# Kernel optimization log

Measured on AMD Instinct MI355X. Metric: run time of the kernel, lower is better.

## Reference

```python
import jax, jax.numpy as jnp
import numpy as np

B, S, H, E, T, L = 128, 1024, 512, 512, 64, 128


def setup_inputs() -> dict:
    key = jax.random.key(0)
    ks = jax.random.split(key, 20)
    s = 0.02
    inp = {
        "sent_lengths": jax.random.randint(ks[0], (B,), 1, S, dtype=jnp.int32),
        "output_length": T,
        "decoder_input": jax.random.normal(ks[1], (B, E), jnp.float32),
        "h0": jax.random.normal(ks[2], (B, H), jnp.float32),
        "c0": jax.random.normal(ks[3], (B, H), jnp.float32),
        "context": jax.random.normal(ks[4], (B, S, H), jnp.float32),
        "cur_labels": jax.random.randint(ks[5], (B, T), 0, L, dtype=jnp.int32),
        "cur_max_nsymbs": jax.random.randint(ks[6], (B,), 0, 10, dtype=jnp.int32),
        # parameters
        "label_emb": jax.random.normal(ks[7], (L, E), jnp.float32) * s,
        "W_ih": jax.random.normal(ks[8], (4 * H, E), jnp.float32) * s,
        "b_ih": jnp.zeros((4 * H,), jnp.float32),
        "W_hh": jax.random.normal(ks[9], (4 * H, H), jnp.float32) * s,
        "b_hh": jnp.zeros((4 * H,), jnp.float32),
        "W_ho": jax.random.normal(ks[10], (H, 2 * H), jnp.float32) * s,
        "b_ho": jnp.zeros((H,), jnp.float32),
        "W_attn_in": jax.random.normal(ks[11], (H, H), jnp.float32) * s,
        "b_attn_in": jnp.zeros((H,), jnp.float32),
        "W_attn_ctx": jax.random.normal(ks[12], (H, H), jnp.float32) * s,
        "b_attn_ctx": jnp.zeros((H,), jnp.float32),
        "V": jax.random.uniform(ks[13], (H,), jnp.float32, -1.0, 1.0),
        "W_out": jax.random.normal(ks[14], (L, 2 * H + E), jnp.float32) * s,
        "b_out": jnp.zeros((L,), jnp.float32),
    }
    # padding_idx row of the label embedding is zero (torch nn.Embedding semantics)
    inp["label_emb"] = inp["label_emb"].at[0].set(0.0)
    return inp


def _decode(output_length, decoder_input, h0, c0, context, cur_labels,
            label_emb, W_ih, b_ih, W_hh, b_hh, W_ho, b_ho,
            W_attn_in, b_attn_in, W_attn_ctx, b_attn_ctx, V, W_out, b_out):
    # Precompute the 1x1-conv context projection once (identical math to per-step conv).
    ctx = jnp.einsum("bsh,gh->bsg", context, W_attn_ctx) + b_attn_ctx  # [B,S,H]

    # Teacher-forced input sequence: x_0 = decoder_input, x_i = emb(labels[:, i-1]).
    emb = label_emb[cur_labels]                     # [B,T,E]
    xs = jnp.concatenate(
        [decoder_input[None], jnp.swapaxes(emb, 0, 1)[: output_length - 1]], axis=0
    )                                               # [T,B,E]

    def step(carry, x):
        h, c = carry
        gates = x @ W_ih.T + b_ih + h @ W_hh.T + b_hh          # [B,4H]
        i_g, f_g, g_g, o_g = jnp.split(gates, 4, axis=1)
        c_t = jax.nn.sigmoid(f_g) * c + jax.nn.sigmoid(i_g) * jnp.tanh(g_g)
        h_lstm = jax.nn.sigmoid(o_g) * jnp.tanh(c_t)            # [B,H]
        # pointer attention
        inp = h_lstm @ W_attn_in.T + b_attn_in                  # [B,H]
        att = jnp.einsum("bsh,h->bs", jnp.tanh(inp[:, None, :] + ctx), V)
        alpha = jax.nn.softmax(att, axis=-1)                    # [B,S]
        weighted = jnp.einsum("bs,bsh->bh", alpha, ctx)         # [B,H]
        hidden_t = jnp.tanh(jnp.concatenate([weighted, h_lstm], 1) @ W_ho.T + b_ho)
        out = jnp.concatenate([hidden_t, weighted, x], 1) @ W_out.T + b_out  # [B,L]
        return (hidden_t, c_t), out

    (h_f, c_f), outs = jax.lax.scan(step, (h0, c0), xs)  # outs [T,B,L]
    outputs = jnp.transpose(outs, (1, 0, 2))             # [B,T,L]
    preds = jnp.argmax(outputs, axis=-1)                 # [B,T]
    return outputs, preds, h_f, c_f


def reference(sent_lengths, output_length, decoder_input, h0, c0, context,
              cur_labels, cur_max_nsymbs, label_emb, W_ih, b_ih, W_hh, b_hh,
              W_ho, b_ho, W_attn_in, b_attn_in, W_attn_ctx, b_attn_ctx, V,
              W_out, b_out):
    # cur_batch_len = len(sent_lengths) == B, so hidden slicing is a no-op here.
    # cur_max_nsymbs unused (constrained_decoding=None path).
    return _decode(output_length, decoder_input, h0, c0, context, cur_labels,
                   label_emb, W_ih, b_ih, W_hh, b_hh, W_ho, b_ho,
                   W_attn_in, b_attn_in, W_attn_ctx, b_attn_ctx, V, W_out, b_out)
```

## Files before the change

kernel.cpp:

```cpp
#include <hip/hip_runtime.h>
#include <hip/hip_bf16.h>
#include <math.h>

#define B_ 128
#define S_ 1024
#define H_ 512
#define E_ 512
#define T_ 64
#define L_ 128
#define G4H 2048

typedef __attribute__((ext_vector_type(8))) short bf16x8;
typedef __attribute__((ext_vector_type(4))) float f32x4;

__device__ inline float sigmoidf_(float x) { return 1.f / (1.f + expf(-x)); }
__device__ inline float fast_tanhf_(float x) {
    float e = __expf(2.f * x);
    return 1.f - 2.f / (e + 1.f);
}
__device__ inline unsigned f2bf1(float f) {
    unsigned u = __float_as_uint(f);
    return (u + 0x7fffu + ((u >> 16) & 1u)) >> 16;
}

#define LDP 40
__global__ __launch_bounds__(256) void gemm_split(
    const float* __restrict__ A, int lda,
    const float* __restrict__ W, int ldw,
    const float* __restrict__ bias,
    const float* __restrict__ Cinit, int ldci,
    float* __restrict__ C, int ldc,
    int K, int act, int perm)
{
    __shared__ unsigned short Ah[128 * LDP];
    __shared__ unsigned short Al[128 * LDP];
    __shared__ unsigned short Bh[128 * LDP];
    __shared__ unsigned short Bl[128 * LDP];
    const int n0 = blockIdx.x * 128;
    const int m0 = blockIdx.y * 128;
    const int t = threadIdx.x;
    const int lane = t & 63, wv = t >> 6;
    const int wr = wv >> 1, wc = wv & 1;
    const int row = t >> 1, koff = (t & 1) * 16;

    f32x4 acc[4][4] = {};

    for (int kt = 0; kt < K; kt += 32) {
        float av[16], wvv[16];
        {
            const float* ap = A + (size_t)(m0 + row) * lda + kt + koff;
            const float* wp = W + (size_t)(n0 + row) * ldw + kt + koff;
#pragma unroll
            for (int q = 0; q < 4; ++q) {
                *reinterpret_cast<float4*>(&av[q * 4]) = *reinterpret_cast<const float4*>(ap + q * 4);
                *reinterpret_cast<float4*>(&wvv[q * 4]) = *reinterpret_cast<const float4*>(wp + q * 4);
            }
        }
        unsigned short ah[16], al[16], bh[16], bl[16];
#pragma unroll
        for (int e = 0; e < 16; ++e) {
            unsigned ha = f2bf1(av[e]);
            float hf = __uint_as_float(ha << 16);
            ah[e] = (unsigned short)ha;
            al[e] = (unsigned short)f2bf1(av[e] - hf);
            unsigned hw = f2bf1(wvv[e]);
            float hwf = __uint_as_float(hw << 16);
            bh[e] = (unsigned short)hw;
            bl[e] = (unsigned short)f2bf1(wvv[e] - hwf);
        }
        __syncthreads();
        *reinterpret_cast<uint4*>(&Ah[row * LDP + koff])     = *reinterpret_cast<uint4*>(&ah[0]);
        *reinterpret_cast<uint4*>(&Ah[row * LDP + koff + 8]) = *reinterpret_cast<uint4*>(&ah[8]);
        *reinterpret_cast<uint4*>(&Al[row * LDP + koff])     = *reinterpret_cast<uint4*>(&al[0]);
        *reinterpret_cast<uint4*>(&Al[row * LDP + koff + 8]) = *reinterpret_cast<uint4*>(&al[8]);
        *reinterpret_cast<uint4*>(&Bh[row * LDP + koff])     = *reinterpret_cast<uint4*>(&bh[0]);
        *reinterpret_cast<uint4*>(&Bh[row * LDP + koff + 8]) = *reinterpret_cast<uint4*>(&bh[8]);
        *reinterpret_cast<uint4*>(&Bl[row * LDP + koff])     = *reinterpret_cast<uint4*>(&bl[0]);
        *reinterpret_cast<uint4*>(&Bl[row * LDP + koff + 8]) = *reinterpret_cast<uint4*>(&bl[8]);
        __syncthreads();

        bf16x8 fah[4], fal[4], fbh[4], fbl[4];
        const int kq = (lane >> 4) * 8;
#pragma unroll
        for (int i = 0; i < 4; ++i) {
            const int ar = wr * 64 + i * 16 + (lane & 15);
            const int br = wc * 64 + i * 16 + (lane & 15);
            fah[i] = *reinterpret_cast<const bf16x8*>(&Ah[ar * LDP + kq]);
            fal[i] = *reinterpret_cast<const bf16x8*>(&Al[ar * LDP + kq]);
            fbh[i] = *reinterpret_cast<const bf16x8*>(&Bh[br * LDP + kq]);
            fbl[i] = *reinterpret_cast<const bf16x8*>(&Bl[br * LDP + kq]);
        }
#pragma unroll
        for (int i = 0; i < 4; ++i)
#pragma unroll
            for (int j = 0; j < 4; ++j) {
                acc[i][j] = __builtin_amdgcn_mfma_f32_16x16x32_bf16(fah[i], fbh[j], acc[i][j], 0, 0, 0);
                acc[i][j] = __builtin_amdgcn_mfma_f32_16x16x32_bf16(fal[i], fbh[j], acc[i][j], 0, 0, 0);
                acc[i][j] = __builtin_amdgcn_mfma_f32_16x16x32_bf16(fah[i], fbl[j], acc[i][j], 0, 0, 0);
            }
    }

#pragma unroll
    for (int i = 0; i < 4; ++i)
#pragma unroll
        for (int j = 0; j < 4; ++j) {
            const int n = n0 + wc * 64 + j * 16 + (lane & 15);
            const float bs = bias ? bias[n] : 0.f;
#pragma unroll
            for (int r = 0; r < 4; ++r) {
                const int m = m0 + wr * 64 + i * 16 + (lane >> 4) * 4 + r;
                float v = acc[i][j][r] + bs;
                if (Cinit) v += Cinit[(size_t)m * ldci + n];
                if (act == 1) v = tanhf(v);
                size_t crow;
                if (perm) { int bb = m & 127, tt = m >> 7; crow = ((size_t)bb * T_ + tt) * ldc; }
                else crow = (size_t)m * ldc;
                C[crow + n] = v;
            }
        }
}

__global__ __launch_bounds__(128) void k_perm(
    const float* __restrict__ W_ih, const float* __restrict__ W_hh,
    const float* __restrict__ b_ih, const float* __restrict__ b_hh,
    float* __restrict__ Wip, float* __restrict__ Whp, float* __restrict__ bp)
{
    int rp = blockIdx.x;
    int h = rp >> 2, g = rp & 3;
    int src = g * 512 + h;
    int t = threadIdx.x;
    const float4* si = reinterpret_cast<const float4*>(W_ih + (size_t)src * 512);
    const float4* sh = reinterpret_cast<const float4*>(W_hh + (size_t)src * 512);
    float4* di = reinterpret_cast<float4*>(Wip + (size_t)rp * 512);
    float4* dh = reinterpret_cast<float4*>(Whp + (size_t)rp * 512);
    di[t] = si[t];
    dh[t] = sh[t];
    if (t == 0) bp[rp] = b_ih[src] + b_hh[src];
}

__global__ __launch_bounds__(256) void k_gateslstm(
    const float* __restrict__ hbuf,
    const float* __restrict__ Whp,
    const float* __restrict__ xproj_t,
    float* __restrict__ cbuf,
    float* __restrict__ hlstm)
{
    __shared__ float As[16][32];
    __shared__ float Ws[16][64];
    const int n0 = blockIdx.x * 64;
    const int m0 = blockIdx.y * 32;
    const int t = threadIdx.x;
    const int tx = t & 15;
    const int ty = t >> 4;
    const int alr = t >> 3, alk = (t & 7) * 2;
    const int wlr = t >> 2, wlk = (t & 3) * 4;

    float acc[2][4] = {};

    for (int k0 = 0; k0 < 512; k0 += 16) {
        float2 a2 = *reinterpret_cast<const float2*>(hbuf + (size_t)(m0 + alr) * 512 + k0 + alk);
        float4 w4 = *reinterpret_cast<const float4*>(Whp + (size_t)(n0 + wlr) * 512 + k0 + wlk);
        __syncthreads();
        As[alk + 0][alr] = a2.x; As[alk + 1][alr] = a2.y;
        Ws[wlk + 0][wlr] = w4.x; Ws[wlk + 1][wlr] = w4.y;
        Ws[wlk + 2][wlr] = w4.z; Ws[wlk + 3][wlr] = w4.w;
        __syncthreads();
#pragma unroll
        for (int kk = 0; kk < 16; ++kk) {
            float a[2], b[4];
            a[0] = As[kk][ty * 2]; a[1] = As[kk][ty * 2 + 1];
#pragma unroll
            for (int j = 0; j < 4; ++j) b[j] = Ws[kk][tx * 4 + j];
#pragma unroll
            for (int i = 0; i < 2; ++i)
#pragma unroll
                for (int j = 0; j < 4; ++j) acc[i][j] = fmaf(a[i], b[j], acc[i][j]);
        }
    }

    const int h = (n0 >> 2) + tx;
#pragma unroll
    for (int i = 0; i < 2; ++i) {
        const int b = m0 + ty * 2 + i;
        float4 xp = *reinterpret_cast<const float4*>(xproj_t + (size_t)b * G4H + n0 + tx * 4);
        float ig = sigmoidf_(acc[i][0] + xp.x);
        float fg = sigmoidf_(acc[i][1] + xp.y);
        float gg = tanhf(acc[i][2] + xp.z);
        float og = sigmoidf_(acc[i][3] + xp.w);
        float c = fg * cbuf[(size_t)b * 512 + h] + ig * gg;
        cbuf[(size_t)b * 512 + h] = c;
        hlstm[(size_t)b * 512 + h] = og * tanhf(c);
    }
}

__global__ __launch_bounds__(256) void gemm_stepk(
    const float* __restrict__ A, int lda,
    const float* __restrict__ W, int ldw,
    float* __restrict__ P, int N, int Kc)
{
    __shared__ float As[16][128];
    __shared__ float Ws[16][64];
    const int n0 = blockIdx.x * 64;
    const int k0 = blockIdx.y * Kc;
    const int t = threadIdx.x;
    const int tx = t & 15;
    const int ty = t >> 4;
    const int ar = t >> 1, akq = (t & 1) * 8;
    const int wr = t >> 2, wkq = (t & 3) * 4;

    float acc[8][4] = {};

    for (int kb = 0; kb < Kc; kb += 16) {
        float4 a0 = *reinterpret_cast<const float4*>(A + (size_t)ar * lda + k0 + kb + akq);
        float4 a1 = *reinterpret_cast<const float4*>(A + (size_t)ar * lda + k0 + kb + akq + 4);
        float4 w0 = *reinterpret_cast<const float4*>(W + (size_t)(n0 + wr) * ldw + k0 + kb + wkq);
        __syncthreads();
        As[akq + 0][ar] = a0.x; As[akq + 1][ar] = a0.y; As[akq + 2][ar] = a0.z; As[akq + 3][ar] = a0.w;
        As[akq + 4][ar] = a1.x; As[akq + 5][ar] = a1.y; As[akq + 6][ar] = a1.z; As[akq + 7][ar] = a1.w;
        Ws[wkq + 0][wr] = w0.x; Ws[wkq + 1][wr] = w0.y; Ws[wkq + 2][wr] = w0.z; Ws[wkq + 3][wr] = w0.w;
        __syncthreads();
#pragma unroll
        for (int kk = 0; kk < 16; ++kk) {
            float a[8], b[4];
#pragma unroll
            for (int i = 0; i < 8; ++i) a[i] = As[kk][ty * 8 + i];
#pragma unroll
            for (int j = 0; j < 4; ++j) b[j] = Ws[kk][tx * 4 + j];
#pragma unroll
            for (int i = 0; i < 8; ++i)
#pragma unroll
                for (int j = 0; j < 4; ++j) acc[i][j] = fmaf(a[i], b[j], acc[i][j]);
        }
    }

#pragma unroll
    for (int i = 0; i < 8; ++i) {
        const int m = ty * 8 + i;
#pragma unroll
        for (int j = 0; j < 4; ++j)
            P[((size_t)blockIdx.y * 128 + m) * N + n0 + tx * 4 + j] = acc[i][j];
    }
}

__global__ __launch_bounds__(256) void k_who(
    const float* __restrict__ pm, const float* __restrict__ pl,
    const float* __restrict__ pw, const float* __restrict__ hlstm,
    const float* __restrict__ W_ho,
    float* __restrict__ P, float* __restrict__ hist_t)
{
    __shared__ float As[16][128];
    __shared__ float Ws[16][64];
    __shared__ float eql[128][4];
    const int n0 = blockIdx.x * 64;
    const int k0 = blockIdx.y * 128;
    const int t = threadIdx.x;
    const int tx = t & 15;
    const int ty = t >> 4;
    const int ar = t >> 1, akq = (t & 1) * 8;
    const int wr = t >> 2, wkq = (t & 3) * 4;
    const bool merge_side = (k0 < 512);
    const bool writer = (blockIdx.x == 0) && merge_side;

    if (merge_side && t < 128) {
        float m0 = pm[4 * t], m1 = pm[4 * t + 1], m2 = pm[4 * t + 2], m3 = pm[4 * t + 3];
        float M = fmaxf(fmaxf(m0, m1), fmaxf(m2, m3));
        float e0 = __expf(m0 - M), e1 = __expf(m1 - M), e2 = __expf(m2 - M), e3 = __expf(m3 - M);
        float Lt = e0 * pl[4 * t] + e1 * pl[4 * t + 1] + e2 * pl[4 * t + 2] + e3 * pl[4 * t + 3];
        float inv = 1.f / Lt;
        eql[t][0] = e0 * inv; eql[t][1] = e1 * inv; eql[t][2] = e2 * inv; eql[t][3] = e3 * inv;
    }
    __syncthreads();

    float acc[8][4] = {};

    for (int kb = 0; kb < 128; kb += 16) {
        float av[8];
        const int kg = k0 + kb + akq;
        if (merge_side) {
            float4 p0a = *reinterpret_cast<const float4*>(pw + ((size_t)(4 * ar + 0) * 512) + kg);
            float4 p0b = *reinterpret_cast<const float4*>(pw + ((size_t)(4 * ar + 0) * 512) + kg + 4);
            float4 p1a = *reinterpret_cast<const float4*>(pw + ((size_t)(4 * ar + 1) * 512) + kg);
            float4 p1b = *reinterpret_cast<const float4*>(pw + ((size_t)(4 * ar + 1) * 512) + kg + 4);
            float4 p2a = *reinterpret_cast<const float4*>(pw + ((size_t)(4 * ar + 2) * 512) + kg);
            float4 p2b = *reinterpret_cast<const float4*>(pw + ((size_t)(4 * ar + 2) * 512) + kg + 4);
            float4 p3a = *reinterpret_cast<const float4*>(pw + ((size_t)(4 * ar + 3) * 512) + kg);
            float4 p3b = *reinterpret_cast<const float4*>(pw + ((size_t)(4 * ar + 3) * 512) + kg + 4);
            float q0 = eql[ar][0], q1 = eql[ar][1], q2 = eql[ar][2], q3 = eql[ar][3];
            av[0] = q0 * p0a.x + q1 * p1a.x + q2 * p2a.x + q3 * p3a.x;
            av[1] = q0 * p0a.y + q1 * p1a.y + q2 * p2a.y + q3 * p3a.y;
            av[2] = q0 * p0a.z + q1 * p1a.z + q2 * p2a.z + q3 * p3a.z;
            av[3] = q0 * p0a.w + q1 * p1a.w + q2 * p2a.w + q3 * p3a.w;
            av[4] = q0 * p0b.x + q1 * p1b.x + q2 * p2b.x + q3 * p3b.x;
            av[5] = q0 * p0b.y + q1 * p1b.y + q2 * p2b.y + q3 * p3b.y;
            av[6] = q0 * p0b.z + q1 * p1b.z + q2 * p2b.z + q3 * p3b.z;
            av[7] = q0 * p0b.w + q1 * p1b.w + q2 * p2b.w + q3 * p3b.w;
            if (writer) {
                *reinterpret_cast<float4*>(hist_t + (size_t)ar * 1024 + 512 + kg) = *reinterpret_cast<float4*>(&av[0]);
                *reinterpret_cast<float4*>(hist_t + (size_t)ar * 1024 + 512 + kg + 4) = *reinterpret_cast<float4*>(&av[4]);
            }
        } else {
            *reinterpret_cast<float4*>(&av[0]) = *reinterpret_cast<const float4*>(hlstm + (size_t)ar * 512 + kg - 512);
            *reinterpret_cast<float4*>(&av[4]) = *reinterpret_cast<const float4*>(hlstm + (size_t)ar * 512 + kg - 512 + 4);
        }
        float4 w0 = *reinterpret_cast<const float4*>(W_ho + (size_t)(n0 + wr) * 1024 + k0 + kb + wkq);
        __syncthreads();
        As[akq + 0][ar] = av[0]; As[akq + 1][ar] = av[1]; As[akq + 2][ar] = av[2]; As[akq + 3][ar] = av[3];
        As[akq + 4][ar] = av[4]; As[akq + 5][ar] = av[5]; As[akq + 6][ar] = av[6]; As[akq + 7][ar] = av[7];
        Ws[wkq + 0][wr] = w0.x; Ws[wkq + 1][wr] = w0.y; Ws[wkq + 2][wr] = w0.z; Ws[wkq + 3][wr] = w0.w;
        __syncthreads();
#pragma unroll
        for (int kk = 0; kk < 16; ++kk) {
            float a[8], b[4];
#pragma unroll
            for (int i = 0; i < 8; ++i) a[i] = As[kk][ty * 8 + i];
#pragma unroll
            for (int j = 0; j < 4; ++j) b[j] = Ws[kk][tx * 4 + j];
#pragma unroll
            for (int i = 0; i < 8; ++i)
#pragma unroll
                for (int j = 0; j < 4; ++j) acc[i][j] = fmaf(a[i], b[j], acc[i][j]);
        }
    }

#pragma unroll
    for (int i = 0; i < 8; ++i) {
        const int m = ty * 8 + i;
#pragma unroll
        for (int j = 0; j < 4; ++j)
            P[((size_t)blockIdx.y * 128 + m) * 512 + n0 + tx * 4 + j] = acc[i][j];
    }
}

__global__ void k_embed(const float* __restrict__ dec_in, const int* __restrict__ labels,
                        const float* __restrict__ emb, float* __restrict__ X)
{
    size_t total = (size_t)T_ * B_ * E_;
    for (size_t i = (size_t)blockIdx.x * blockDim.x + threadIdx.x; i < total;
         i += (size_t)gridDim.x * blockDim.x) {
        int e = (int)(i % E_);
        int b = (int)((i / E_) % B_);
        int t = (int)(i / ((size_t)E_ * B_));
        float v;
        if (t == 0) v = dec_in[b * E_ + e];
        else {
            int lab = labels[b * T_ + (t - 1)];
            v = emb[(size_t)lab * E_ + e];
        }
        X[i] = v;
    }
}

__global__ void k_init(const float* __restrict__ h0, const float* __restrict__ c0,
                       float* __restrict__ hbuf, float* __restrict__ cbuf)
{
    int i = blockIdx.x * blockDim.x + threadIdx.x;
    hbuf[i] = h0[i];
    cbuf[i] = c0[i];
}

__global__ __launch_bounds__(512) void k_attn(const float* __restrict__ ctx,
    const float* __restrict__ Pa, const float* __restrict__ b_ain,
    const float* __restrict__ Vv,
    float* __restrict__ pm, float* __restrict__ pl, float* __restrict__ pw)
{
    int blk = blockIdx.x;
    int b = blk >> 2, q = blk & 3;
    int tid = threadIdx.x, lane = tid & 63, wv = tid >> 6;

    __shared__ float inp_sh[512];
    inp_sh[tid] = Pa[(size_t)b * 512 + tid]
                + Pa[(size_t)(128 + b) * 512 + tid]
                + Pa[(size_t)(256 + b) * 512 + tid]
                + Pa[(size_t)(384 + b) * 512 + tid]
                + b_ain[tid];
    __syncthreads();

    float inpr[8], vr[8];
    {
        const float4* v4 = reinterpret_cast<const float4*>(Vv) + lane * 2;
        *(float4*)&vr[0] = v4[0];   *(float4*)&vr[4] = v4[1];
#pragma unroll
        for (int k = 0; k < 8; ++k) inpr[k] = inp_sh[lane * 8 + k];
    }
    const float* cbase = ctx + (size_t)b * S_ * H_ + (size_t)(q * 256) * H_;

    float m = -INFINITY, l = 0.f, w[8] = {};
    for (int si = 0; si < 32; ++si) {
        int s = wv * 32 + si;
        const float4* cp = reinterpret_cast<const float4*>(cbase + (size_t)s * H_) + lane * 2;
        float c8[8];
        *(float4*)&c8[0] = cp[0]; *(float4*)&c8[4] = cp[1];
        float t = 0.f;
#pragma unroll
        for (int k = 0; k < 8; ++k) t = fmaf(fast_tanhf_(inpr[k] + c8[k]), vr[k], t);
#pragma unroll
        for (int off = 32; off > 0; off >>= 1) t += __shfl_xor(t, off);
        float mn = fmaxf(m, t);
        float sc = __expf(m - mn);
        float p  = __expf(t - mn);
        l = l * sc + p;
#pragma unroll
        for (int k = 0; k < 8; ++k) w[k] = w[k] * sc + p * c8[k];
        m = mn;
    }

    __shared__ float wl[8 * 512];
    __shared__ float ml[8], ll[8];
#pragma unroll
    for (int k = 0; k < 8; ++k) wl[wv * 512 + lane * 8 + k] = w[k];
    if (lane == 0) { ml[wv] = m; ll[wv] = l; }
    __syncthreads();

    float M = ml[0];
#pragma unroll
    for (int u = 1; u < 8; ++u) M = fmaxf(M, ml[u]);
    float lt = 0.f, wt = 0.f;
#pragma unroll
    for (int u = 0; u < 8; ++u) {
        float e = __expf(ml[u] - M);
        lt += e * ll[u];
        wt += e * wl[u * 512 + tid];
    }
    if (tid == 0) { pm[blk] = M; pl[blk] = lt; }
    pw[(size_t)blk * 512 + tid] = wt;
}

__global__ __launch_bounds__(256) void k_whofin(const float* __restrict__ Po,
    const float* __restrict__ b_ho, float* __restrict__ hbuf, float* __restrict__ hist_t)
{
    int i = blockIdx.x * blockDim.x + threadIdx.x;
    int b = i >> 9, h = i & 511;
    float v = b_ho[h];
#pragma unroll
    for (int ks = 0; ks < 8; ++ks) v += Po[((size_t)ks * 128 + b) * 512 + h];
    v = tanhf(v);
    hbuf[i] = v;
    hist_t[(size_t)b * 1024 + h] = v;
}

__global__ __launch_bounds__(128) void k_argmax(const float* __restrict__ outp,
                                                float* __restrict__ preds)
{
    int row = blockIdx.x;
    int tid = threadIdx.x;
    float v = outp[(size_t)row * L_ + tid];
    int idx = tid;
#pragma unroll
    for (int off = 32; off > 0; off >>= 1) {
        float ov = __shfl_xor(v, off);
        int oi = __shfl_xor(idx, off);
        if (ov > v || (ov == v && oi < idx)) { v = ov; idx = oi; }
    }
    __shared__ float sv[2];
    __shared__ int si[2];
    if ((tid & 63) == 0) { sv[tid >> 6] = v; si[tid >> 6] = idx; }
    __syncthreads();
    if (tid == 0) {
        float v0 = sv[0], v1 = sv[1];
        int i0 = si[0], i1 = si[1];
        int r = (v1 > v0 || (v1 == v0 && i1 < i0)) ? i1 : i0;
        preds[row] = (float)r;
    }
}

__global__ void k_final(const float* __restrict__ hbuf, const float* __restrict__ cbuf,
                        float* __restrict__ hf, float* __restrict__ cf)
{
    int i = blockIdx.x * blockDim.x + threadIdx.x;
    hf[i] = hbuf[i];
    cf[i] = cbuf[i];
}

extern "C" void kernel_launch(void* const* d_in, const int* in_sizes, int n_in,
                              void* d_out, int out_size, void* d_ws, size_t ws_size,
                              hipStream_t stream)
{
    const float* dec_in  = (const float*)d_in[2];
    const float* h0      = (const float*)d_in[3];
    const float* c0      = (const float*)d_in[4];
    const float* context = (const float*)d_in[5];
    const int*   labels  = (const int*)d_in[6];
    const float* emb     = (const float*)d_in[8];
    const float* W_ih    = (const float*)d_in[9];
    const float* b_ih    = (const float*)d_in[10];
    const float* W_hh    = (const float*)d_in[11];
    const float* b_hh    = (const float*)d_in[12];
    const float* W_ho    = (const float*)d_in[13];
    const float* b_ho    = (const float*)d_in[14];
    const float* W_ain   = (const float*)d_in[15];
    const float* b_ain   = (const float*)d_in[16];
    const float* W_actx  = (const float*)d_in[17];
    const float* b_actx  = (const float*)d_in[18];
    const float* Vv      = (const float*)d_in[19];
    const float* W_out   = (const float*)d_in[20];
    const float* b_out   = (const float*)d_in[21];

    float* ws = (float*)d_ws;
    float* X     = ws; ws += (size_t)T_ * B_ * E_;
    float* xproj = ws; ws += (size_t)T_ * B_ * G4H;
    float* xout  = ws; ws += (size_t)T_ * B_ * L_;
    float* ctx   = ws; ws += (size_t)B_ * S_ * H_;
    float* hist  = ws; ws += (size_t)T_ * B_ * 1024;
    float* Wip   = ws; ws += (size_t)G4H * 512;
    float* Whp   = ws; ws += (size_t)G4H * 512;
    float* bp    = ws; ws += G4H;
    float* Pa    = ws; ws += (size_t)4 * B_ * H_;
    float* Po    = ws; ws += (size_t)8 * B_ * H_;
    float* cbuf  = ws; ws += (size_t)B_ * H_;
    float* hbuf  = ws; ws += (size_t)B_ * H_;
    float* hlstm = ws; ws += (size_t)B_ * H_;
    float* pm    = ws; ws += 512;
    float* pl    = ws; ws += 512;
    float* pw    = ws; ws += (size_t)512 * 512;

    float* out_logits = (float*)d_out;
    float* out_preds  = out_logits + (size_t)B_ * T_ * L_;
    float* out_hf     = out_preds + (size_t)B_ * T_;
    float* out_cf     = out_hf + (size_t)B_ * H_;

    k_embed<<<2048, 256, 0, stream>>>(dec_in, labels, emb, X);
    k_init<<<256, 256, 0, stream>>>(h0, c0, hbuf, cbuf);
    k_perm<<<G4H, 128, 0, stream>>>(W_ih, W_hh, b_ih, b_hh, Wip, Whp, bp);
    gemm_split<<<dim3(16, 64), 256, 0, stream>>>(X, E_, Wip, E_, bp, nullptr, 0,
                                                 xproj, G4H, E_, 0, 0);
    gemm_split<<<dim3(1, 64), 256, 0, stream>>>(X, E_, W_out + 1024, 1536, b_out, nullptr, 0,
                                                xout, L_, E_, 0, 0);
    gemm_split<<<dim3(4, 1024), 256, 0, stream>>>(context, H_, W_actx, H_, b_actx, nullptr, 0,
                                                  ctx, H_, H_, 0, 0);

    for (int t = 0; t < T_; ++t) {
        float* hist_t = hist + (size_t)t * B_ * 1024;
        k_gateslstm<<<dim3(32, 4), 256, 0, stream>>>(hbuf, Whp,
                                                     xproj + (size_t)t * B_ * G4H,
                                                     cbuf, hlstm);
        gemm_stepk<<<dim3(8, 4), 256, 0, stream>>>(hlstm, H_, W_ain, H_, Pa, H_, 128);
        k_attn<<<512, 512, 0, stream>>>(ctx, Pa, b_ain, Vv, pm, pl, pw);
        k_who<<<dim3(8, 8), 256, 0, stream>>>(pm, pl, pw, hlstm, W_ho, Po, hist_t);
        k_whofin<<<256, 256, 0, stream>>>(Po, b_ho, hbuf, hist_t);
    }

    gemm_split<<<dim3(1, 64), 256, 0, stream>>>(hist, 1024, W_out, 1536, nullptr,
                                                xout, L_, out_logits, L_, 1024, 0, 1);
    k_argmax<<<B_ * T_, 128, 0, stream>>>(out_logits, out_preds);
    k_final<<<256, 256, 0, stream>>>(hbuf, cbuf, out_hf, out_cf);
}
```

Baseline: 8.182 ms.

## Register-prefetch next tiles in GEMMs and split attention into eight S-chunks

Adds register double-buffering to gemm_split, the LSTM gates kernel, gemm_stepk and k_who, so the global loads for the next K tile are issued before the current tile's compute. The attention kernel is split into 8 sequence chunks per batch row instead of 4, giving 1024 blocks with 16 positions per wave and a prefetch of the next context row. The W_ho merge side now combines 8 partial softmax results, and the workspace buffers are resized to match. In exchange there is more partial-result traffic and merge work in k_who, plus higher register pressure from the prefetched values.

```diff
diff --git a/kernel.cpp b/kernel.cpp
--- a/kernel.cpp
+++ b/kernel.cpp
@@ -9,6 +9,7 @@
 #define T_ 64
 #define L_ 128
 #define G4H 2048
+#define QS 8
 
 typedef __attribute__((ext_vector_type(8))) short bf16x8;
 typedef __attribute__((ext_vector_type(4))) float f32x4;
@@ -45,17 +46,18 @@
 
     f32x4 acc[4][4] = {};
 
+    float av[16], wvv[16];
+    {
+        const float* ap = A + (size_t)(m0 + row) * lda + koff;
+        const float* wp = W + (size_t)(n0 + row) * ldw + koff;
+#pragma unroll
+        for (int q = 0; q < 4; ++q) {
+            *reinterpret_cast<float4*>(&av[q * 4]) = *reinterpret_cast<const float4*>(ap + q * 4);
+            *reinterpret_cast<float4*>(&wvv[q * 4]) = *reinterpret_cast<const float4*>(wp + q * 4);
+        }
+    }
+
     for (int kt = 0; kt < K; kt += 32) {
-        float av[16], wvv[16];
-        {
-            const float* ap = A + (size_t)(m0 + row) * lda + kt + koff;
-            const float* wp = W + (size_t)(n0 + row) * ldw + kt + koff;
-#pragma unroll
-            for (int q = 0; q < 4; ++q) {
-                *reinterpret_cast<float4*>(&av[q * 4]) = *reinterpret_cast<const float4*>(ap + q * 4);
-                *reinterpret_cast<float4*>(&wvv[q * 4]) = *reinterpret_cast<const float4*>(wp + q * 4);
-            }
-        }
         unsigned short ah[16], al[16], bh[16], bl[16];
 #pragma unroll
         for (int e = 0; e < 16; ++e) {
@@ -78,6 +80,16 @@
         *reinterpret_cast<uint4*>(&Bl[row * LDP + koff])     = *reinterpret_cast<uint4*>(&bl[0]);
         *reinterpret_cast<uint4*>(&Bl[row * LDP + koff + 8]) = *reinterpret_cast<uint4*>(&bl[8]);
         __syncthreads();
+
+        if (kt + 32 < K) {
+            const float* ap = A + (size_t)(m0 + row) * lda + kt + 32 + koff;
+            const float* wp = W + (size_t)(n0 + row) * ldw + kt + 32 + koff;
+#pragma unroll
+            for (int q = 0; q < 4; ++q) {
+                *reinterpret_cast<float4*>(&av[q * 4]) = *reinterpret_cast<const float4*>(ap + q * 4);
+                *reinterpret_cast<float4*>(&wvv[q * 4]) = *reinterpret_cast<const float4*>(wp + q * 4);
+            }
+        }
 
         bf16x8 fah[4], fal[4], fbh[4], fbl[4];
         const int kq = (lane >> 4) * 8;
@@ -157,14 +169,19 @@
 
     float acc[2][4] = {};
 
+    float2 pa = *reinterpret_cast<const float2*>(hbuf + (size_t)(m0 + alr) * 512 + alk);
+    float4 pv = *reinterpret_cast<const float4*>(Whp + (size_t)(n0 + wlr) * 512 + wlk);
+
     for (int k0 = 0; k0 < 512; k0 += 16) {
-        float2 a2 = *reinterpret_cast<const float2*>(hbuf + (size_t)(m0 + alr) * 512 + k0 + alk);
-        float4 w4 = *reinterpret_cast<const float4*>(Whp + (size_t)(n0 + wlr) * 512 + k0 + wlk);
-        __syncthreads();
-        As[alk + 0][alr] = a2.x; As[alk + 1][alr] = a2.y;
-        Ws[wlk + 0][wlr] = w4.x; Ws[wlk + 1][wlr] = w4.y;
-        Ws[wlk + 2][wlr] = w4.z; Ws[wlk + 3][wlr] = w4.w;
-        __syncthreads();
+        __syncthreads();
+        As[alk + 0][alr] = pa.x; As[alk + 1][alr] = pa.y;
+        Ws[wlk + 0][wlr] = pv.x; Ws[wlk + 1][wlr] = pv.y;
+        Ws[wlk + 2][wlr] = pv.z; Ws[wlk + 3][wlr] = pv.w;
+        __syncthreads();
+        if (k0 + 16 < 512) {
+            pa = *reinterpret_cast<const float2*>(hbuf + (size_t)(m0 + alr) * 512 + k0 + 16 + alk);
+            pv = *reinterpret_cast<const float4*>(Whp + (size_t)(n0 + wlr) * 512 + k0 + 16 + wlk);
+        }
 #pragma unroll
         for (int kk = 0; kk < 16; ++kk) {
             float a[2], b[4];
@@ -210,15 +227,21 @@
 
     float acc[8][4] = {};
 
+    float4 a0 = *reinterpret_cast<const float4*>(A + (size_t)ar * lda + k0 + akq);
+    float4 a1 = *reinterpret_cast<const float4*>(A + (size_t)ar * lda + k0 + akq + 4);
+    float4 w0 = *reinterpret_cast<const float4*>(W + (size_t)(n0 + wr) * ldw + k0 + wkq);
+
     for (int kb = 0; kb < Kc; kb += 16) {
-        float4 a0 = *reinterpret_cast<const float4*>(A + (size_t)ar * lda + k0 + kb + akq);
-        float4 a1 = *reinterpret_cast<const float4*>(A + (size_t)ar * lda + k0 + kb + akq + 4);
-        float4 w0 = *reinterpret_cast<const float4*>(W + (size_t)(n0 + wr) * ldw + k0 + kb + wkq);
         __syncthreads();
         As[akq + 0][ar] = a0.x; As[akq + 1][ar] = a0.y; As[akq + 2][ar] = a0.z; As[akq + 3][ar] = a0.w;
         As[akq + 4][ar] = a1.x; As[akq + 5][ar] = a1.y; As[akq + 6][ar] = a1.z; As[akq + 7][ar] = a1.w;
         Ws[wkq + 0][wr] = w0.x; Ws[wkq + 1][wr] = w0.y; Ws[wkq + 2][wr] = w0.z; Ws[wkq + 3][wr] = w0.w;
         __syncthreads();
+        if (kb + 16 < Kc) {
+            a0 = *reinterpret_cast<const float4*>(A + (size_t)ar * lda + k0 + kb + 16 + akq);
+            a1 = *reinterpret_cast<const float4*>(A + (size_t)ar * lda + k0 + kb + 16 + akq + 4);
+            w0 = *reinterpret_cast<const float4*>(W + (size_t)(n0 + wr) * ldw + k0 + kb + 16 + wkq);
+        }
 #pragma unroll
         for (int kk = 0; kk < 16; ++kk) {
             float a[8], b[4];
@@ -250,7 +273,7 @@
 {
     __shared__ float As[16][128];
     __shared__ float Ws[16][64];
-    __shared__ float eql[128][4];
+    __shared__ float eql[128][QS];
     const int n0 = blockIdx.x * 64;
     const int k0 = blockIdx.y * 128;
     const int t = threadIdx.x;
@@ -262,38 +285,39 @@
     const bool writer = (blockIdx.x == 0) && merge_side;
 
     if (merge_side && t < 128) {
-        float m0 = pm[4 * t], m1 = pm[4 * t + 1], m2 = pm[4 * t + 2], m3 = pm[4 * t + 3];
-        float M = fmaxf(fmaxf(m0, m1), fmaxf(m2, m3));
-        float e0 = __expf(m0 - M), e1 = __expf(m1 - M), e2 = __expf(m2 - M), e3 = __expf(m3 - M);
-        float Lt = e0 * pl[4 * t] + e1 * pl[4 * t + 1] + e2 * pl[4 * t + 2] + e3 * pl[4 * t + 3];
+        float mq[QS], eq[QS];
+        float M = -INFINITY;
+#pragma unroll
+        for (int q = 0; q < QS; ++q) { mq[q] = pm[QS * t + q]; M = fmaxf(M, mq[q]); }
+        float Lt = 0.f;
+#pragma unroll
+        for (int q = 0; q < QS; ++q) { eq[q] = __expf(mq[q] - M); Lt += eq[q] * pl[QS * t + q]; }
         float inv = 1.f / Lt;
-        eql[t][0] = e0 * inv; eql[t][1] = e1 * inv; eql[t][2] = e2 * inv; eql[t][3] = e3 * inv;
+#pragma unroll
+        for (int q = 0; q < QS; ++q) eql[t][q] = eq[q] * inv;
     }
     __syncthreads();
 
     float acc[8][4] = {};
-
-    for (int kb = 0; kb < 128; kb += 16) {
-        float av[8];
+    float av[8];
+    float4 w0;
+
+    auto load_stage = [&](int kb) {
         const int kg = k0 + kb + akq;
         if (merge_side) {
-            float4 p0a = *reinterpret_cast<const float4*>(pw + ((size_t)(4 * ar + 0) * 512) + kg);
-            float4 p0b = *reinterpret_cast<const float4*>(pw + ((size_t)(4 * ar + 0) * 512) + kg + 4);
-            float4 p1a = *reinterpret_cast<const float4*>(pw + ((size_t)(4 * ar + 1) * 512) + kg);
-            float4 p1b = *reinterpret_cast<const float4*>(pw + ((size_t)(4 * ar + 1) * 512) + kg + 4);
-            float4 p2a = *reinterpret_cast<const float4*>(pw + ((size_t)(4 * ar + 2) * 512) + kg);
-            float4 p2b = *reinterpret_cast<const float4*>(pw + ((size_t)(4 * ar + 2) * 512) + kg + 4);
-            float4 p3a = *reinterpret_cast<const float4*>(pw + ((size_t)(4 * ar + 3) * 512) + kg);
-            float4 p3b = *reinterpret_cast<const float4*>(pw + ((size_t)(4 * ar + 3) * 512) + kg + 4);
-            float q0 = eql[ar][0], q1 = eql[ar][1], q2 = eql[ar][2], q3 = eql[ar][3];
-            av[0] = q0 * p0a.x + q1 * p1a.x + q2 * p2a.x + q3 * p3a.x;
-            av[1] = q0 * p0a.y + q1 * p1a.y + q2 * p2a.y + q3 * p3a.y;
-            av[2] = q0 * p0a.z + q1 * p1a.z + q2 * p2a.z + q3 * p3a.z;
-            av[3] = q0 * p0a.w + q1 * p1a.w + q2 * p2a.w + q3 * p3a.w;
-            av[4] = q0 * p0b.x + q1 * p1b.x + q2 * p2b.x + q3 * p3b.x;
-            av[5] = q0 * p0b.y + q1 * p1b.y + q2 * p2b.y + q3 * p3b.y;
-            av[6] = q0 * p0b.z + q1 * p1b.z + q2 * p2b.z + q3 * p3b.z;
-            av[7] = q0 * p0b.w + q1 * p1b.w + q2 * p2b.w + q3 * p3b.w;
+#pragma unroll
+            for (int e = 0; e < 8; ++e) av[e] = 0.f;
+#pragma unroll
+            for (int q = 0; q < QS; ++q) {
+                const float* pr = pw + (size_t)(QS * ar + q) * 512 + kg;
+                float4 pa = *reinterpret_cast<const float4*>(pr);
+                float4 pb = *reinterpret_cast<const float4*>(pr + 4);
+                float qw = eql[ar][q];
+                av[0] = fmaf(qw, pa.x, av[0]); av[1] = fmaf(qw, pa.y, av[1]);
+                av[2] = fmaf(qw, pa.z, av[2]); av[3] = fmaf(qw, pa.w, av[3]);
+                av[4] = fmaf(qw, pb.x, av[4]); av[5] = fmaf(qw, pb.y, av[5]);
+                av[6] = fmaf(qw, pb.z, av[6]); av[7] = fmaf(qw, pb.w, av[7]);
+            }
             if (writer) {
                 *reinterpret_cast<float4*>(hist_t + (size_t)ar * 1024 + 512 + kg) = *reinterpret_cast<float4*>(&av[0]);
                 *reinterpret_cast<float4*>(hist_t + (size_t)ar * 1024 + 512 + kg + 4) = *reinterpret_cast<float4*>(&av[4]);
@@ -302,12 +326,18 @@
             *reinterpret_cast<float4*>(&av[0]) = *reinterpret_cast<const float4*>(hlstm + (size_t)ar * 512 + kg - 512);
             *reinterpret_cast<float4*>(&av[4]) = *reinterpret_cast<const float4*>(hlstm + (size_t)ar * 512 + kg - 512 + 4);
         }
-        float4 w0 = *reinterpret_cast<const float4*>(W_ho + (size_t)(n0 + wr) * 1024 + k0 + kb + wkq);
+        w0 = *reinterpret_cast<const float4*>(W_ho + (size_t)(n0 + wr) * 1024 + k0 + kb + wkq);
+    };
+
+    load_stage(0);
+
+    for (int kb = 0; kb < 128; kb += 16) {
         __syncthreads();
         As[akq + 0][ar] = av[0]; As[akq + 1][ar] = av[1]; As[akq + 2][ar] = av[2]; As[akq + 3][ar] = av[3];
         As[akq + 4][ar] = av[4]; As[akq + 5][ar] = av[5]; As[akq + 6][ar] = av[6]; As[akq + 7][ar] = av[7];
         Ws[wkq + 0][wr] = w0.x; Ws[wkq + 1][wr] = w0.y; Ws[wkq + 2][wr] = w0.z; Ws[wkq + 3][wr] = w0.w;
         __syncthreads();
+        if (kb + 16 < 128) load_stage(kb + 16);
 #pragma unroll
         for (int kk = 0; kk < 16; ++kk) {
             float a[8], b[4];
@@ -364,7 +394,7 @@
     float* __restrict__ pm, float* __restrict__ pl, float* __restrict__ pw)
 {
     int blk = blockIdx.x;
-    int b = blk >> 2, q = blk & 3;
+    int b = blk >> 3, q = blk & 7;
     int tid = threadIdx.x, lane = tid & 63, wv = tid >> 6;
 
     __shared__ float inp_sh[512];
@@ -382,14 +412,19 @@
 #pragma unroll
         for (int k = 0; k < 8; ++k) inpr[k] = inp_sh[lane * 8 + k];
     }
-    const float* cbase = ctx + (size_t)b * S_ * H_ + (size_t)(q * 256) * H_;
+    const float* sp = ctx + ((size_t)b * S_ + q * 128 + wv * 16) * H_ + lane * 8;
 
     float m = -INFINITY, l = 0.f, w[8] = {};
-    for (int si = 0; si < 32; ++si) {
-        int s = wv * 32 + si;
-        const float4* cp = reinterpret_cast<const float4*>(cbase + (size_t)s * H_) + lane * 2;
+    float4 c0 = *reinterpret_cast<const float4*>(sp);
+    float4 c1 = *reinterpret_cast<const float4*>(sp + 4);
+    for (int si = 0; si < 16; ++si) {
+        float4 u0 = c0, u1 = c1;
+        if (si < 15) {
+            c0 = *reinterpret_cast<const float4*>(sp + (size_t)(si + 1) * H_);
+            c1 = *reinterpret_cast<const float4*>(sp + (size_t)(si + 1) * H_ + 4);
+        }
         float c8[8];
-        *(float4*)&c8[0] = cp[0]; *(float4*)&c8[4] = cp[1];
+        *(float4*)&c8[0] = u0; *(float4*)&c8[4] = u1;
         float t = 0.f;
 #pragma unroll
         for (int k = 0; k < 8; ++k) t = fmaf(fast_tanhf_(inpr[k] + c8[k]), vr[k], t);
@@ -509,9 +544,9 @@
     float* cbuf  = ws; ws += (size_t)B_ * H_;
     float* hbuf  = ws; ws += (size_t)B_ * H_;
     float* hlstm = ws; ws += (size_t)B_ * H_;
-    float* pm    = ws; ws += 512;
-    float* pl    = ws; ws += 512;
-    float* pw    = ws; ws += (size_t)512 * 512;
+    float* pm    = ws; ws += (size_t)B_ * QS;
+    float* pl    = ws; ws += (size_t)B_ * QS;
+    float* pw    = ws; ws += (size_t)B_ * QS * 512;
 
     float* out_logits = (float*)d_out;
     float* out_preds  = out_logits + (size_t)B_ * T_ * L_;
@@ -534,7 +569,7 @@
                                                      xproj + (size_t)t * B_ * G4H,
                                                      cbuf, hlstm);
         gemm_stepk<<<dim3(8, 4), 256, 0, stream>>>(hlstm, H_, W_ain, H_, Pa, H_, 128);
-        k_attn<<<512, 512, 0, stream>>>(ctx, Pa, b_ain, Vv, pm, pl, pw);
+        k_attn<<<B_ * QS, 512, 0, stream>>>(ctx, Pa, b_ain, Vv, pm, pl, pw);
         k_who<<<dim3(8, 8), 256, 0, stream>>>(pm, pl, pw, hlstm, W_ho, Po, hist_t);
         k_whofin<<<256, 256, 0, stream>>>(Po, b_ho, hbuf, hist_t);
     }
```

Measured after the change: 7.470 ms. -8.7%, faster.
